# Kernel tuning notes

Measured on AMD Instinct MI355X. Metric: run time of the kernel, lower is better.

## Reference

```python
import jax, jax.numpy as jnp
import numpy as np

D = 1024
H = 16
HD = D // H
EPS = 1e-8


def setup_inputs() -> dict:
    key = jax.random.key(0)
    ks = jax.random.split(key, 12)
    B, S = 2, 2048
    scale = 1.0 / np.sqrt(D)
    inp = {
        "x": jax.random.normal(ks[0], (B, S, D), dtype=jnp.float32),
        "M": jax.random.uniform(ks[1], (B, S, S), dtype=jnp.float32),
        "Wq": jax.random.normal(ks[2], (D, D), dtype=jnp.float32) * scale,
        "bq": jax.random.normal(ks[3], (D,), dtype=jnp.float32) * 0.01,
        "Wk": jax.random.normal(ks[4], (D, D), dtype=jnp.float32) * scale,
        "bk": jax.random.normal(ks[5], (D,), dtype=jnp.float32) * 0.01,
        "Wv": jax.random.normal(ks[6], (D, D), dtype=jnp.float32) * scale,
        "bv": jax.random.normal(ks[7], (D,), dtype=jnp.float32) * 0.01,
        "Wo": jax.random.normal(ks[8], (D, D), dtype=jnp.float32) * scale,
        "bo": jax.random.normal(ks[9], (D,), dtype=jnp.float32) * 0.01,
    }
    return inp


def reference(x, M, Wq, bq, Wk, bk, Wv, bv, Wo, bo):
    B, S, _ = x.shape
    sm_scale = HD ** -0.5
    # projections (torch Linear: x @ W^T + b), split into heads: [B,H,S,HD]
    def proj(W, b):
        return (x @ W.T + b).reshape(B, S, H, HD).transpose(0, 2, 1, 3)
    Q, K, V = proj(Wq, bq), proj(Wk, bk), proj(Wv, bv)
    # scores: [B,H,S,S], gated pre-softmax by M broadcast over heads
    scores = jnp.einsum("bhqd,bhkd->bhqk", Q, K) * sm_scale
    Mb = M[:, None, :, :]  # [B,1,S,S]
    scores = scores * Mb
    attn = jax.nn.softmax(scores, axis=-1)
    # post-softmax re-gate + L1 renormalize
    A_sparse = attn * Mb
    norm = jnp.sum(jnp.abs(A_sparse), axis=-1, keepdims=True) + EPS
    A_bar = A_sparse / norm
    out = jnp.einsum("bhqk,bhkd->bhqd", A_bar, V)
    out = out.transpose(0, 2, 1, 3).reshape(B, S, D)
    return out @ Wo.T + bo
```

## Files before the change

### kernel.cpp

```cpp
#include <hip/hip_runtime.h>
#include <hip/hip_bf16.h>
#include <stdint.h>

#define S_LEN 2048
#define D_DIM 1024
#define NROW 4096

typedef __attribute__((ext_vector_type(8))) short short8;
typedef __attribute__((ext_vector_type(4))) float f32x4;
typedef __attribute__((ext_vector_type(4))) int i32x4;
typedef __attribute__((ext_vector_type(8))) _Float16 h8;
typedef unsigned short ushort_t;

__device__ __forceinline__ ushort_t f2bf(float f) {
  uint32_t u = __float_as_uint(f);
  u += 0x7fffu + ((u >> 16) & 1u);
  return (ushort_t)(u >> 16);
}

__device__ __forceinline__ ushort_t f2h(float f) {
  _Float16 h = (_Float16)f;
  return __builtin_bit_cast(ushort_t, h);
}

__device__ __forceinline__ void gload16(const void* g, void* l) {
  __builtin_amdgcn_global_load_lds((const __attribute__((address_space(1))) void*)g,
                                   (__attribute__((address_space(3))) void*)l, 16, 0, 0);
}

__global__ void convert4_kernel(const float* __restrict__ x,
                                const float* __restrict__ wq, const float* __restrict__ wk,
                                const float* __restrict__ wv,
                                ushort_t* __restrict__ xb, ushort_t* __restrict__ wcat) {
  const float* src; ushort_t* dst; int n;
  switch (blockIdx.y) {
    case 0: src = x;  dst = xb;             n = NROW * D_DIM;  break;
    case 1: src = wq; dst = wcat;           n = D_DIM * D_DIM; break;
    case 2: src = wk; dst = wcat + 1048576; n = D_DIM * D_DIM; break;
    default: src = wv; dst = wcat + 2097152; n = D_DIM * D_DIM; break;
  }
  int base = (blockIdx.x * 256 + threadIdx.x) * 8;
  if (base >= n) return;
  f32x4 va = *(const f32x4*)(src + base);
  f32x4 vb = *(const f32x4*)(src + base + 4);
  short8 o;
  o[0] = (short)f2bf(va[0]); o[1] = (short)f2bf(va[1]);
  o[2] = (short)f2bf(va[2]); o[3] = (short)f2bf(va[3]);
  o[4] = (short)f2bf(vb[0]); o[5] = (short)f2bf(vb[1]);
  o[6] = (short)f2bf(vb[2]); o[7] = (short)f2bf(vb[3]);
  *(short8*)(dst + base) = o;
}

__global__ void convert_wo_kernel(const float* __restrict__ wo, ushort_t* __restrict__ wob) {
  int base = (blockIdx.x * 256 + threadIdx.x) * 8;
  f32x4 va = *(const f32x4*)(wo + base);
  f32x4 vb = *(const f32x4*)(wo + base + 4);
  short8 o;
  o[0] = (short)f2bf(va[0]); o[1] = (short)f2bf(va[1]);
  o[2] = (short)f2bf(va[2]); o[3] = (short)f2bf(va[3]);
  o[4] = (short)f2bf(vb[0]); o[5] = (short)f2bf(vb[1]);
  o[6] = (short)f2bf(vb[2]); o[7] = (short)f2bf(vb[3]);
  *(short8*)(wob + base) = o;
}

__global__ __launch_bounds__(256) void m2_transform(const float* __restrict__ M,
                                                    ushort_t* __restrict__ M2) {
  int tid = blockIdx.x * 256 + threadIdx.x;
  int lane = tid & 63, w = (tid >> 6) & 7, kt = (tid >> 9) & 31, combo = tid >> 14;
  int c0 = lane & 15, g = lane >> 4;
  int b = combo >> 4, q0i = combo & 15;
  const float* src = M + ((size_t)b * 2048 + q0i * 128 + w * 16 + c0) * 2048 + kt * 64 + g * 4;
  ushort_t outv[16];
#pragma unroll
  for (int nf = 0; nf < 4; ++nf) {
    f32x4 v = *(const f32x4*)(src + nf * 16);
#pragma unroll
    for (int r = 0; r < 4; ++r)
      outv[nf * 4 + r] = f2h(v[r]);
  }
  *(short8*)(M2 + (size_t)tid * 16)     = *(short8*)&outv[0];
  *(short8*)(M2 + (size_t)tid * 16 + 8) = *(short8*)&outv[8];
}

template<int MODE>
__global__ __launch_bounds__(256, 4) void gemm_glds(const ushort_t* __restrict__ A,
                                                    const ushort_t* __restrict__ Bw,
                                                    const float* __restrict__ bias0,
                                                    const float* __restrict__ bias1,
                                                    const float* __restrict__ bias2,
                                                    void* __restrict__ Cout) {
  __shared__ ushort_t As[128 * 64];
  __shared__ ushort_t Bs[128 * 64];
  const int t = threadIdx.x;
  const int lane = t & 63;
  const int w = t >> 6;
  const int wm = w >> 1, wn = w & 1;
  const int m0 = blockIdx.x * 128, n0 = blockIdx.y * 128;
  const int g = lane >> 4, c0 = lane & 15;
  const int srow = lane >> 3, scol = (lane & 7) * 8;

  f32x4 acc[4][4] = {};

  for (int kt = 0; kt < 16; ++kt) {
    const int kk = kt * 64;
#pragma unroll
    for (int i = 0; i < 4; ++i) {
      gload16(A  + (size_t)(m0 + w * 32 + i * 8 + srow) * D_DIM + kk + scol, &As[(w * 32 + i * 8) * 64]);
      gload16(Bw + (size_t)(n0 + w * 32 + i * 8 + srow) * D_DIM + kk + scol, &Bs[(w * 32 + i * 8) * 64]);
    }
    asm volatile("s_waitcnt vmcnt(0)" ::: "memory");
    __syncthreads();
#pragma unroll
    for (int kc = 0; kc < 2; ++kc) {
      short8 af[4], bf[4];
#pragma unroll
      for (int mf = 0; mf < 4; ++mf)
        af[mf] = *(const short8*)&As[(wm * 64 + mf * 16 + c0) * 64 + kc * 32 + g * 8];
#pragma unroll
      for (int nf = 0; nf < 4; ++nf)
        bf[nf] = *(const short8*)&Bs[(wn * 64 + nf * 16 + c0) * 64 + kc * 32 + g * 8];
#pragma unroll
      for (int mf = 0; mf < 4; ++mf)
#pragma unroll
        for (int nf = 0; nf < 4; ++nf)
          acc[mf][nf] = __builtin_amdgcn_mfma_f32_16x16x32_bf16(af[mf], bf[nf], acc[mf][nf], 0, 0, 0);
    }
    __syncthreads();
  }

#pragma unroll
  for (int nf = 0; nf < 4; ++nf) {
    int jj = n0 + wn * 64 + nf * 16 + c0;
    float bval;
    if (MODE == 0) {
      int proj = jj >> 10, jcol = jj & 1023;
      const float* bp = (proj == 0) ? bias0 : ((proj == 1) ? bias1 : bias2);
      bval = bp[jcol];
    } else {
      bval = bias0[jj];
    }
#pragma unroll
    for (int mf = 0; mf < 4; ++mf) {
#pragma unroll
      for (int r = 0; r < 4; ++r) {
        int ii = m0 + wm * 64 + mf * 16 + g * 4 + r;
        float v = acc[mf][nf][r] + bval;
        if (MODE == 2) {
          ((float*)Cout)[(size_t)ii * D_DIM + jj] = v;
        } else {
          int proj = jj >> 10, jcol = jj & 1023;
          if (proj == 0) v *= 0.125f;
          int bb = ii >> 11, s = ii & 2047;
          size_t addr;
          if (proj < 2) {
            int hcol = jcol >> 6, hd = jcol & 63;
            addr = (size_t)proj * 4194304 + ((size_t)(bb * 16 + hcol) * 2048 + s) * 64 + hd;
          } else {
            addr = (size_t)2 * 4194304 + ((size_t)bb * 1024 + jcol) * 2048 + s;
          }
          ((ushort_t*)Cout)[addr] = f2bf(v);
        }
      }
    }
  }
}

__global__ __launch_bounds__(512, 4) void attn_kernel(const ushort_t* __restrict__ Qg,
                                                      const ushort_t* __restrict__ Kg,
                                                      const ushort_t* __restrict__ Vtg,
                                                      const ushort_t* __restrict__ M2,
                                                      ushort_t* __restrict__ aout) {
  __shared__ ushort_t Ks[2][64 * 72];
  __shared__ ushort_t Vts[2][64 * 72];

  const int t = threadIdx.x, lane = t & 63, w = t >> 6;
  const int g = lane >> 4, c0 = lane & 15;
  const int id = blockIdx.x;
  const int r8 = id & 7, hh = (id >> 3) & 15, ss = id >> 7;
  const int combo = r8 + 8 * ss, b = combo >> 4, q0 = (combo & 15) * 128;
  const int bh = b * 16 + hh;

  const ushort_t* Qbase  = Qg  + ((size_t)bh * 2048 + q0) * 64;
  const ushort_t* Kbase  = Kg  + (size_t)bh * 2048 * 64;
  const ushort_t* Vtbase = Vtg + (size_t)bh * 64 * 2048;
  const ushort_t* M2base = M2 + ((size_t)combo * 32 * 8 + w) * 64 * 16 + (size_t)lane * 16;

  short8 qf[2];
#pragma unroll
  for (int kc = 0; kc < 2; ++kc)
    qf[kc] = *(const short8*)(Qbase + (size_t)(w * 16 + c0) * 64 + kc * 32 + g * 8);

  f32x4 o[4] = {};
  float dpe = 0.f;
  const int idxA = (((g & 1) * 2 + (g >> 1)) * 16 + c0) * 4;
  const int idxB = (((g & 1) * 2 + 1 - (g >> 1)) * 16 + c0) * 4;
  const bool glo = (g < 2);
  const bool gb = (g & 1);

  const int srow = t >> 3, sc8 = (t & 7) * 8;
  short8 rk, rv, rm0, rm1, rm0n, rm1n;

  rk  = *(const short8*)(Kbase + (size_t)srow * 64 + sc8);
  rv  = *(const short8*)(Vtbase + (size_t)srow * 2048 + sc8);
  rm0 = *(const short8*)(M2base);
  rm1 = *(const short8*)(M2base + 8);
  *(short8*)&Ks[0][srow * 72 + sc8]  = rk;
  *(short8*)&Vts[0][srow * 72 + sc8] = rv;
  __syncthreads();

  for (int kt = 0; kt < 32; ++kt) {
    const int cur = kt & 1;
    if (kt < 31) {
      const int k0 = (kt + 1) * 64;
      rk  = *(const short8*)(Kbase + (size_t)(k0 + srow) * 64 + sc8);
      rv  = *(const short8*)(Vtbase + (size_t)srow * 2048 + k0 + sc8);
      rm0n = *(const short8*)(M2base + (size_t)(kt + 1) * 8192);
      rm1n = *(const short8*)(M2base + (size_t)(kt + 1) * 8192 + 8);
    }

    f32x4 sf[4] = {};
#pragma unroll
    for (int kc = 0; kc < 2; ++kc) {
      short8 kf[4];
#pragma unroll
      for (int nf = 0; nf < 4; ++nf)
        kf[nf] = *(const short8*)&Ks[cur][(nf * 16 + c0) * 72 + kc * 32 + g * 8];
#pragma unroll
      for (int nf = 0; nf < 4; ++nf)
        sf[nf] = __builtin_amdgcn_mfma_f32_16x16x32_bf16(kf[nf], qf[kc], sf[nf], 0, 0, 0);
    }

    h8 mh0 = __builtin_bit_cast(h8, rm0);
    h8 mh1 = __builtin_bit_cast(h8, rm1);
    uint32_t w4[4][2];
#pragma unroll
    for (int nf = 0; nf < 4; ++nf) {
      float p[4];
#pragma unroll
      for (int r = 0; r < 4; ++r) {
        float m = (nf < 2) ? (float)mh0[nf * 4 + r] : (float)mh1[(nf - 2) * 4 + r];
        float e = __expf(sf[nf][r] * m);
        float pe = m * e;
        dpe += pe;
        p[r] = pe;
      }
      asm("v_cvt_pk_bf16_f32 %0, %1, %2" : "=v"(w4[nf][0]) : "v"(p[0]), "v"(p[1]));
      asm("v_cvt_pk_bf16_f32 %0, %1, %2" : "=v"(w4[nf][1]) : "v"(p[2]), "v"(p[3]));
    }

    short8 pf[2];
#pragma unroll
    for (int kc = 0; kc < 2; ++kc) {
      uint32_t sA0 = gb ? w4[2 * kc + 1][0] : w4[2 * kc][0];
      uint32_t sA1 = gb ? w4[2 * kc + 1][1] : w4[2 * kc][1];
      uint32_t sB0 = gb ? w4[2 * kc][0]     : w4[2 * kc + 1][0];
      uint32_t sB1 = gb ? w4[2 * kc][1]     : w4[2 * kc + 1][1];
      uint32_t rA0 = (uint32_t)__builtin_amdgcn_ds_bpermute(idxA, (int)sA0);
      uint32_t rA1 = (uint32_t)__builtin_amdgcn_ds_bpermute(idxA, (int)sA1);
      uint32_t rB0 = (uint32_t)__builtin_amdgcn_ds_bpermute(idxB, (int)sB0);
      uint32_t rB1 = (uint32_t)__builtin_amdgcn_ds_bpermute(idxB, (int)sB1);
      i32x4 f4;
      f4[0] = (int)(glo ? rA0 : rB0);
      f4[1] = (int)(glo ? rA1 : rB1);
      f4[2] = (int)(glo ? rB0 : rA0);
      f4[3] = (int)(glo ? rB1 : rA1);
      pf[kc] = __builtin_bit_cast(short8, f4);
    }

#pragma unroll
    for (int kc = 0; kc < 2; ++kc) {
#pragma unroll
      for (int df = 0; df < 4; ++df) {
        short8 vf = *(const short8*)&Vts[cur][(df * 16 + c0) * 72 + kc * 32 + g * 8];
        o[df] = __builtin_amdgcn_mfma_f32_16x16x32_bf16(vf, pf[kc], o[df], 0, 0, 0);
      }
    }

    if (kt < 31) {
      *(short8*)&Ks[cur ^ 1][srow * 72 + sc8]  = rk;
      *(short8*)&Vts[cur ^ 1][srow * 72 + sc8] = rv;
      rm0 = rm0n; rm1 = rm1n;
    }
    __syncthreads();
  }

  dpe += __shfl_xor(dpe, 16);
  dpe += __shfl_xor(dpe, 32);
  float inv = 1.0f / dpe;

#pragma unroll
  for (int df = 0; df < 4; ++df) {
    float v0 = o[df][0] * inv, v1 = o[df][1] * inv;
    float v2 = o[df][2] * inv, v3 = o[df][3] * inv;
    uint32_t d0, d1;
    asm("v_cvt_pk_bf16_f32 %0, %1, %2" : "=v"(d0) : "v"(v0), "v"(v1));
    asm("v_cvt_pk_bf16_f32 %0, %1, %2" : "=v"(d1) : "v"(v2), "v"(v3));
    unsigned long long pk = (unsigned long long)d0 | ((unsigned long long)d1 << 32);
    *(unsigned long long*)&aout[((size_t)b * 2048 + q0 + w * 16 + c0) * 1024 + hh * 64 + df * 16 + g * 4] = pk;
  }
}

extern "C" void kernel_launch(void* const* d_in, const int* in_sizes, int n_in,
                              void* d_out, int out_size, void* d_ws, size_t ws_size,
                              hipStream_t stream) {
  const float* x  = (const float*)d_in[0];
  const float* M  = (const float*)d_in[1];
  const float* Wq = (const float*)d_in[2];
  const float* bq = (const float*)d_in[3];
  const float* Wk = (const float*)d_in[4];
  const float* bk = (const float*)d_in[5];
  const float* Wv = (const float*)d_in[6];
  const float* bv = (const float*)d_in[7];
  const float* Wo = (const float*)d_in[8];
  const float* bo = (const float*)d_in[9];
  float* out = (float*)d_out;
  char* ws = (char*)d_ws;

  ushort_t* Qb    = (ushort_t*)(ws);
  ushort_t* Kb    = (ushort_t*)(ws + 8388608);
  ushort_t* Vtb   = (ushort_t*)(ws + 16777216);
  ushort_t* xb    = (ushort_t*)(ws + 25165824);
  ushort_t* Wcat  = (ushort_t*)(ws + 33554432);
  ushort_t* M2    = (ushort_t*)(ws + 25165824);
  ushort_t* aoutb = (ushort_t*)(ws + 41943040);
  ushort_t* wob   = (ushort_t*)(ws);

  convert4_kernel<<<dim3(2048, 4), 256, 0, stream>>>(x, Wq, Wk, Wv, xb, Wcat);
  gemm_glds<0><<<dim3(32, 24), 256, 0, stream>>>(xb, Wcat, bq, bk, bv, (void*)Qb);
  m2_transform<<<2048, 256, 0, stream>>>(M, M2);
  attn_kernel<<<512, 512, 0, stream>>>(Qb, Kb, Vtb, M2, aoutb);
  convert_wo_kernel<<<512, 256, 0, stream>>>(Wo, wob);
  gemm_glds<2><<<dim3(32, 8), 256, 0, stream>>>(aoutb, wob, bo, bo, bo, (void*)out);
}
```

Measured before the change: 151.9 us.

## Fuse mask conversion into attention and shrink attention blocks to 64 query rows

Drops the separate m2_transform kernel that converted M to fp16 in a fragment-friendly layout. The attention kernel now reads fp32 M directly per key tile. The attention grid is re-tiled from 512 blocks of 512 threads (128 query rows) to 1024 blocks of 256 threads (64 query rows), and the K/V shared buffer goes from double-buffered to single-buffered with an extra barrier. The intent is to remove one kernel launch plus the write and re-read of M2, and to raise occupancy. The cost is that every head block re-reads the full fp32 M row from memory (16 heads reuse it, hopefully from L2), and single buffering may serialize loads and compute.

```diff
diff --git a/kernel.cpp b/kernel.cpp
--- a/kernel.cpp
+++ b/kernel.cpp
@@ -9,18 +9,12 @@
 typedef __attribute__((ext_vector_type(8))) short short8;
 typedef __attribute__((ext_vector_type(4))) float f32x4;
 typedef __attribute__((ext_vector_type(4))) int i32x4;
-typedef __attribute__((ext_vector_type(8))) _Float16 h8;
 typedef unsigned short ushort_t;
 
 __device__ __forceinline__ ushort_t f2bf(float f) {
   uint32_t u = __float_as_uint(f);
   u += 0x7fffu + ((u >> 16) & 1u);
   return (ushort_t)(u >> 16);
-}
-
-__device__ __forceinline__ ushort_t f2h(float f) {
-  _Float16 h = (_Float16)f;
-  return __builtin_bit_cast(ushort_t, h);
 }
 
 __device__ __forceinline__ void gload16(const void* g, void* l) {
@@ -61,25 +55,6 @@
   o[4] = (short)f2bf(vb[0]); o[5] = (short)f2bf(vb[1]);
   o[6] = (short)f2bf(vb[2]); o[7] = (short)f2bf(vb[3]);
   *(short8*)(wob + base) = o;
-}
-
-__global__ __launch_bounds__(256) void m2_transform(const float* __restrict__ M,
-                                                    ushort_t* __restrict__ M2) {
-  int tid = blockIdx.x * 256 + threadIdx.x;
-  int lane = tid & 63, w = (tid >> 6) & 7, kt = (tid >> 9) & 31, combo = tid >> 14;
-  int c0 = lane & 15, g = lane >> 4;
-  int b = combo >> 4, q0i = combo & 15;
-  const float* src = M + ((size_t)b * 2048 + q0i * 128 + w * 16 + c0) * 2048 + kt * 64 + g * 4;
-  ushort_t outv[16];
-#pragma unroll
-  for (int nf = 0; nf < 4; ++nf) {
-    f32x4 v = *(const f32x4*)(src + nf * 16);
-#pragma unroll
-    for (int r = 0; r < 4; ++r)
-      outv[nf * 4 + r] = f2h(v[r]);
-  }
-  *(short8*)(M2 + (size_t)tid * 16)     = *(short8*)&outv[0];
-  *(short8*)(M2 + (size_t)tid * 16 + 8) = *(short8*)&outv[8];
 }
 
 template<int MODE>
@@ -165,25 +140,27 @@
   }
 }
 
-__global__ __launch_bounds__(512, 4) void attn_kernel(const ushort_t* __restrict__ Qg,
+__global__ __launch_bounds__(256, 4) void attn_kernel(const ushort_t* __restrict__ Qg,
                                                       const ushort_t* __restrict__ Kg,
                                                       const ushort_t* __restrict__ Vtg,
-                                                      const ushort_t* __restrict__ M2,
+                                                      const float* __restrict__ Mg,
                                                       ushort_t* __restrict__ aout) {
-  __shared__ ushort_t Ks[2][64 * 72];
-  __shared__ ushort_t Vts[2][64 * 72];
+  __shared__ ushort_t Ks[64 * 72];
+  __shared__ ushort_t Vts[64 * 72];
 
   const int t = threadIdx.x, lane = t & 63, w = t >> 6;
   const int g = lane >> 4, c0 = lane & 15;
   const int id = blockIdx.x;
-  const int r8 = id & 7, hh = (id >> 3) & 15, ss = id >> 7;
-  const int combo = r8 + 8 * ss, b = combo >> 4, q0 = (combo & 15) * 128;
+  const int xcd = id & 7, j = id >> 3;
+  const int hh = j & 15, gi = j >> 4;
+  const int g64 = xcd + 8 * gi;
+  const int b = g64 >> 5, q0 = (g64 & 31) * 64;
   const int bh = b * 16 + hh;
 
   const ushort_t* Qbase  = Qg  + ((size_t)bh * 2048 + q0) * 64;
   const ushort_t* Kbase  = Kg  + (size_t)bh * 2048 * 64;
   const ushort_t* Vtbase = Vtg + (size_t)bh * 64 * 2048;
-  const ushort_t* M2base = M2 + ((size_t)combo * 32 * 8 + w) * 64 * 16 + (size_t)lane * 16;
+  const float*    Mbase  = Mg + ((size_t)b * 2048 + q0 + w * 16 + c0) * 2048 + g * 4;
 
   short8 qf[2];
 #pragma unroll
@@ -197,25 +174,27 @@
   const bool glo = (g < 2);
   const bool gb = (g & 1);
 
-  const int srow = t >> 3, sc8 = (t & 7) * 8;
-  short8 rk, rv, rm0, rm1, rm0n, rm1n;
-
-  rk  = *(const short8*)(Kbase + (size_t)srow * 64 + sc8);
-  rv  = *(const short8*)(Vtbase + (size_t)srow * 2048 + sc8);
-  rm0 = *(const short8*)(M2base);
-  rm1 = *(const short8*)(M2base + 8);
-  *(short8*)&Ks[0][srow * 72 + sc8]  = rk;
-  *(short8*)&Vts[0][srow * 72 + sc8] = rv;
-  __syncthreads();
+  short8 rk[2], rv[2];
+#define A_LOAD(kt) { const int k0 = (kt) * 64; \
+    _Pragma("unroll") for (int i = 0; i < 2; ++i) { int c = i * 256 + t; int row = c >> 3, c8 = (c & 7) * 8; \
+      rk[i] = *(const short8*)(Kbase  + (size_t)(k0 + row) * 64 + c8); \
+      rv[i] = *(const short8*)(Vtbase + (size_t)row * 2048 + k0 + c8); } }
+#define A_WRITE() { \
+    _Pragma("unroll") for (int i = 0; i < 2; ++i) { int c = i * 256 + t; int row = c >> 3, c8 = (c & 7) * 8; \
+      *(short8*)&Ks[row * 72 + c8]  = rk[i]; \
+      *(short8*)&Vts[row * 72 + c8] = rv[i]; } }
+
+  A_LOAD(0); A_WRITE(); __syncthreads();
 
   for (int kt = 0; kt < 32; ++kt) {
-    const int cur = kt & 1;
-    if (kt < 31) {
-      const int k0 = (kt + 1) * 64;
-      rk  = *(const short8*)(Kbase + (size_t)(k0 + srow) * 64 + sc8);
-      rv  = *(const short8*)(Vtbase + (size_t)srow * 2048 + k0 + sc8);
-      rm0n = *(const short8*)(M2base + (size_t)(kt + 1) * 8192);
-      rm1n = *(const short8*)(M2base + (size_t)(kt + 1) * 8192 + 8);
+    if (kt < 31) A_LOAD(kt + 1);
+
+    f32x4 mv[4];
+    {
+      const float* Mk = Mbase + kt * 64;
+#pragma unroll
+      for (int nf = 0; nf < 4; ++nf)
+        mv[nf] = *(const f32x4*)(Mk + nf * 16);
     }
 
     f32x4 sf[4] = {};
@@ -224,21 +203,19 @@
       short8 kf[4];
 #pragma unroll
       for (int nf = 0; nf < 4; ++nf)
-        kf[nf] = *(const short8*)&Ks[cur][(nf * 16 + c0) * 72 + kc * 32 + g * 8];
+        kf[nf] = *(const short8*)&Ks[(nf * 16 + c0) * 72 + kc * 32 + g * 8];
 #pragma unroll
       for (int nf = 0; nf < 4; ++nf)
         sf[nf] = __builtin_amdgcn_mfma_f32_16x16x32_bf16(kf[nf], qf[kc], sf[nf], 0, 0, 0);
     }
 
-    h8 mh0 = __builtin_bit_cast(h8, rm0);
-    h8 mh1 = __builtin_bit_cast(h8, rm1);
     uint32_t w4[4][2];
 #pragma unroll
     for (int nf = 0; nf < 4; ++nf) {
       float p[4];
 #pragma unroll
       for (int r = 0; r < 4; ++r) {
-        float m = (nf < 2) ? (float)mh0[nf * 4 + r] : (float)mh1[(nf - 2) * 4 + r];
+        float m = mv[nf][r];
         float e = __expf(sf[nf][r] * m);
         float pe = m * e;
         dpe += pe;
@@ -271,17 +248,16 @@
     for (int kc = 0; kc < 2; ++kc) {
 #pragma unroll
       for (int df = 0; df < 4; ++df) {
-        short8 vf = *(const short8*)&Vts[cur][(df * 16 + c0) * 72 + kc * 32 + g * 8];
+        short8 vf = *(const short8*)&Vts[(df * 16 + c0) * 72 + kc * 32 + g * 8];
         o[df] = __builtin_amdgcn_mfma_f32_16x16x32_bf16(vf, pf[kc], o[df], 0, 0, 0);
       }
     }
 
+    __syncthreads();
     if (kt < 31) {
-      *(short8*)&Ks[cur ^ 1][srow * 72 + sc8]  = rk;
-      *(short8*)&Vts[cur ^ 1][srow * 72 + sc8] = rv;
-      rm0 = rm0n; rm1 = rm1n;
-    }
-    __syncthreads();
+      A_WRITE();
+      __syncthreads();
+    }
   }
 
   dpe += __shfl_xor(dpe, 16);
@@ -298,6 +274,8 @@
     unsigned long long pk = (unsigned long long)d0 | ((unsigned long long)d1 << 32);
     *(unsigned long long*)&aout[((size_t)b * 2048 + q0 + w * 16 + c0) * 1024 + hh * 64 + df * 16 + g * 4] = pk;
   }
+#undef A_LOAD
+#undef A_WRITE
 }
 
 extern "C" void kernel_launch(void* const* d_in, const int* in_sizes, int n_in,
@@ -321,14 +299,12 @@
   ushort_t* Vtb   = (ushort_t*)(ws + 16777216);
   ushort_t* xb    = (ushort_t*)(ws + 25165824);
   ushort_t* Wcat  = (ushort_t*)(ws + 33554432);
-  ushort_t* M2    = (ushort_t*)(ws + 25165824);
   ushort_t* aoutb = (ushort_t*)(ws + 41943040);
-  ushort_t* wob   = (ushort_t*)(ws);
+  ushort_t* wob   = (ushort_t*)(ws + 39845888);
 
   convert4_kernel<<<dim3(2048, 4), 256, 0, stream>>>(x, Wq, Wk, Wv, xb, Wcat);
+  convert_wo_kernel<<<512, 256, 0, stream>>>(Wo, wob);
   gemm_glds<0><<<dim3(32, 24), 256, 0, stream>>>(xb, Wcat, bq, bk, bv, (void*)Qb);
-  m2_transform<<<2048, 256, 0, stream>>>(M, M2);
-  attn_kernel<<<512, 512, 0, stream>>>(Qb, Kb, Vtb, M2, aoutb);
-  convert_wo_kernel<<<512, 256, 0, stream>>>(Wo, wob);
+  attn_kernel<<<1024, 256, 0, stream>>>(Qb, Kb, Vtb, M, aoutb);
   gemm_glds<2><<<dim3(32, 8), 256, 0, stream>>>(aoutb, wob, bo, bo, bo, (void*)out);
 }
```

Result: slower. 158.4 us (+4.3%).

## Process two K/V tiles per iteration with four-slot LDS ring buffer

Applied to the files above, without the earlier changes.

The attention loop now processes two 64-key tiles per iteration. It uses a four-slot LDS ring and prefetches the next two tiles' K, V and mask into registers. This halves the number of block barriers and deepens the prefetch. In exchange it doubles LDS use per block and raises register pressure, which can lower the number of resident blocks per CU. An unused COMPUTE_TILE macro is also defined.

```diff
diff --git a/kernel.cpp b/kernel.cpp
--- a/kernel.cpp
+++ b/kernel.cpp
@@ -170,8 +170,8 @@
                                                       const ushort_t* __restrict__ Vtg,
                                                       const ushort_t* __restrict__ M2,
                                                       ushort_t* __restrict__ aout) {
-  __shared__ ushort_t Ks[2][64 * 72];
-  __shared__ ushort_t Vts[2][64 * 72];
+  __shared__ ushort_t Ks[4][64 * 72];
+  __shared__ ushort_t Vts[4][64 * 72];
 
   const int t = threadIdx.x, lane = t & 63, w = t >> 6;
   const int g = lane >> 4, c0 = lane & 15;
@@ -198,88 +198,151 @@
   const bool gb = (g & 1);
 
   const int srow = t >> 3, sc8 = (t & 7) * 8;
-  short8 rk, rv, rm0, rm1, rm0n, rm1n;
-
-  rk  = *(const short8*)(Kbase + (size_t)srow * 64 + sc8);
-  rv  = *(const short8*)(Vtbase + (size_t)srow * 2048 + sc8);
-  rm0 = *(const short8*)(M2base);
-  rm1 = *(const short8*)(M2base + 8);
-  *(short8*)&Ks[0][srow * 72 + sc8]  = rk;
-  *(short8*)&Vts[0][srow * 72 + sc8] = rv;
+
+#define COMPUTE_TILE(bidx, RM0, RM1) { \
+    f32x4 sf[4] = {}; \
+    _Pragma("unroll") for (int kc = 0; kc < 2; ++kc) { \
+      short8 kf[4]; \
+      _Pragma("unroll") for (int nf = 0; nf < 4; ++nf) \
+        kf[nf] = *(const short8*)&Ks[bidx][(nf * 16 + c0) * 72 + kc * 32 + g * 8]; \
+      _Pragma("unroll") for (int nf = 0; nf < 4; ++nf) \
+        sf[nf] = __builtin_amdgcn_mfma_f32_16x16x32_bf16(kf[nf], qf[kc], sf[nf], 0, 0, 0); \
+    } \
+    h8 mh0 = __builtin_bit_cast(h8, RM0); \
+    h8 mh1 = __builtin_bit_cast(h8, RM1); \
+    uint32_t w4[4][2]; \
+    _Pragma("unroll") for (int nf = 0; nf < 4; ++nf) { \
+      float p[4]; \
+      _Pragma("unroll") for (int r = 0; r < 4; ++r) { \
+        float m = (nf < 2) ? (float)mh0[nf * 4 + r] : (float)mh1[(nf - 2) * 4 + r]; \
+        float e = __expf(sf[nf][r] * m); \
+        float pe = m * e; \
+        dpe += pe; \
+        p[r] = pe; \
+      } \
+      asm("v_cvt_pk_bf16_f32 %0, %1, %2" : "=v"(w4[nf][0]) : "v"(p[0]), "v"(p[1])); \
+      asm("v_cvt_pk_bf16_f32 %0, %1, %2" : "=v"(w4[nf][1]) : "v"(p[2]), "v"(p[3])); \
+    } \
+    short8 pf[2]; \
+    _Pragma("unroll") for (int kc = 0; kc < 2; ++kc) { \
+      uint32_t sA0 = gb ? w4[2 * kc + 1][0] : w4[2 * kc][0]; \
+      uint32_t sA1 = gb ? w4[2 * kc + 1][1] : w4[2 * kc][1]; \
+      uint32_t sB0 = gb ? w4[2 * kc][0]     : w4[2 * kc + 1][0]; \
+      uint32_t sB1 = gb ? w4[2 * kc][1]     : w4[2 * kc + 1][1]; \
+      uint32_t rA0 = (uint32_t)__builtin_amdgcn_ds_bpermute(idxA, (int)sA0); \
+      uint32_t rA1 = (uint32_t)__builtin_amdgcn_ds_bpermute(idxA, (int)sA1); \
+      uint32_t rB0 = (uint32_t)__builtin_amdgcn_ds_bpermute(idxB, (int)sB0); \
+      uint32_t rB1 = (uint32_t)__builtin_amdgcn_ds_bpermute(idxB, (int)sB1); \
+      i32x4 f4; \
+      f4[0] = (int)(glo ? rA0 : rB0); \
+      f4[1] = (int)(glo ? rA1 : rB1); \
+      f4[2] = (int)(glo ? rB0 : rA0); \
+      f4[3] = (int)(glo ? rB1 : rA1); \
+      pf[kc] = __builtin_bit_cast(short8, f4); \
+    } \
+    _Pragma("unroll") for (int kc = 0; kc < 2; ++kc) { \
+      _Pragma("unroll") for (int df = 0; df < 4; ++df) { \
+        short8 vf = *(const short8*)&Vts[bidx][(df * 16 + c0) * 72 + kc * 32 + g * 8]; \
+        o[df] = __builtin_amdgcn_mfma_f32_16x16x32_bf16(vf, pf[kc], o[df], 0, 0, 0); \
+      } \
+    } }
+
+  short8 rmA0, rmA1, rmB0, rmB1;
+  {
+    short8 k0 = *(const short8*)(Kbase + (size_t)srow * 64 + sc8);
+    short8 v0 = *(const short8*)(Vtbase + (size_t)srow * 2048 + sc8);
+    short8 k1 = *(const short8*)(Kbase + (size_t)(64 + srow) * 64 + sc8);
+    short8 v1 = *(const short8*)(Vtbase + (size_t)srow * 2048 + 64 + sc8);
+    *(short8*)&Ks[0][srow * 72 + sc8]  = k0;
+    *(short8*)&Vts[0][srow * 72 + sc8] = v0;
+    *(short8*)&Ks[1][srow * 72 + sc8]  = k1;
+    *(short8*)&Vts[1][srow * 72 + sc8] = v1;
+    rmA0 = *(const short8*)(M2base);
+    rmA1 = *(const short8*)(M2base + 8);
+    rmB0 = *(const short8*)(M2base + 8192);
+    rmB1 = *(const short8*)(M2base + 8192 + 8);
+  }
   __syncthreads();
 
-  for (int kt = 0; kt < 32; ++kt) {
-    const int cur = kt & 1;
-    if (kt < 31) {
-      const int k0 = (kt + 1) * 64;
-      rk  = *(const short8*)(Kbase + (size_t)(k0 + srow) * 64 + sc8);
-      rv  = *(const short8*)(Vtbase + (size_t)srow * 2048 + k0 + sc8);
-      rm0n = *(const short8*)(M2base + (size_t)(kt + 1) * 8192);
-      rm1n = *(const short8*)(M2base + (size_t)(kt + 1) * 8192 + 8);
-    }
-
-    f32x4 sf[4] = {};
-#pragma unroll
-    for (int kc = 0; kc < 2; ++kc) {
-      short8 kf[4];
-#pragma unroll
-      for (int nf = 0; nf < 4; ++nf)
-        kf[nf] = *(const short8*)&Ks[cur][(nf * 16 + c0) * 72 + kc * 32 + g * 8];
-#pragma unroll
-      for (int nf = 0; nf < 4; ++nf)
-        sf[nf] = __builtin_amdgcn_mfma_f32_16x16x32_bf16(kf[nf], qf[kc], sf[nf], 0, 0, 0);
-    }
-
-    h8 mh0 = __builtin_bit_cast(h8, rm0);
-    h8 mh1 = __builtin_bit_cast(h8, rm1);
-    uint32_t w4[4][2];
-#pragma unroll
-    for (int nf = 0; nf < 4; ++nf) {
-      float p[4];
-#pragma unroll
-      for (int r = 0; r < 4; ++r) {
-        float m = (nf < 2) ? (float)mh0[nf * 4 + r] : (float)mh1[(nf - 2) * 4 + r];
-        float e = __expf(sf[nf][r] * m);
-        float pe = m * e;
-        dpe += pe;
-        p[r] = pe;
-      }
-      asm("v_cvt_pk_bf16_f32 %0, %1, %2" : "=v"(w4[nf][0]) : "v"(p[0]), "v"(p[1]));
-      asm("v_cvt_pk_bf16_f32 %0, %1, %2" : "=v"(w4[nf][1]) : "v"(p[2]), "v"(p[3]));
-    }
-
-    short8 pf[2];
-#pragma unroll
-    for (int kc = 0; kc < 2; ++kc) {
-      uint32_t sA0 = gb ? w4[2 * kc + 1][0] : w4[2 * kc][0];
-      uint32_t sA1 = gb ? w4[2 * kc + 1][1] : w4[2 * kc][1];
-      uint32_t sB0 = gb ? w4[2 * kc][0]     : w4[2 * kc + 1][0];
-      uint32_t sB1 = gb ? w4[2 * kc][1]     : w4[2 * kc + 1][1];
-      uint32_t rA0 = (uint32_t)__builtin_amdgcn_ds_bpermute(idxA, (int)sA0);
-      uint32_t rA1 = (uint32_t)__builtin_amdgcn_ds_bpermute(idxA, (int)sA1);
-      uint32_t rB0 = (uint32_t)__builtin_amdgcn_ds_bpermute(idxB, (int)sB0);
-      uint32_t rB1 = (uint32_t)__builtin_amdgcn_ds_bpermute(idxB, (int)sB1);
-      i32x4 f4;
-      f4[0] = (int)(glo ? rA0 : rB0);
-      f4[1] = (int)(glo ? rA1 : rB1);
-      f4[2] = (int)(glo ? rB0 : rA0);
-      f4[3] = (int)(glo ? rB1 : rA1);
-      pf[kc] = __builtin_bit_cast(short8, f4);
-    }
-
-#pragma unroll
-    for (int kc = 0; kc < 2; ++kc) {
-#pragma unroll
-      for (int df = 0; df < 4; ++df) {
-        short8 vf = *(const short8*)&Vts[cur][(df * 16 + c0) * 72 + kc * 32 + g * 8];
-        o[df] = __builtin_amdgcn_mfma_f32_16x16x32_bf16(vf, pf[kc], o[df], 0, 0, 0);
-      }
-    }
-
-    if (kt < 31) {
-      *(short8*)&Ks[cur ^ 1][srow * 72 + sc8]  = rk;
-      *(short8*)&Vts[cur ^ 1][srow * 72 + sc8] = rv;
-      rm0 = rm0n; rm1 = rm1n;
+  for (int kt = 0; kt < 32; kt += 2) {
+    short8 rk2, rv2, rk3, rv3, rmA0n, rmA1n, rmB0n, rmB1n;
+    if (kt < 30) {
+      const int k2 = (kt + 2) * 64, k3 = (kt + 3) * 64;
+      rk2 = *(const short8*)(Kbase + (size_t)(k2 + srow) * 64 + sc8);
+      rv2 = *(const short8*)(Vtbase + (size_t)srow * 2048 + k2 + sc8);
+      rk3 = *(const short8*)(Kbase + (size_t)(k3 + srow) * 64 + sc8);
+      rv3 = *(const short8*)(Vtbase + (size_t)srow * 2048 + k3 + sc8);
+      rmA0n = *(const short8*)(M2base + (size_t)(kt + 2) * 8192);
+      rmA1n = *(const short8*)(M2base + (size_t)(kt + 2) * 8192 + 8);
+      rmB0n = *(const short8*)(M2base + (size_t)(kt + 3) * 8192);
+      rmB1n = *(const short8*)(M2base + (size_t)(kt + 3) * 8192 + 8);
+    }
+
+    ushort_t* KsA = &Ks[kt & 3][0];
+    ushort_t* VtA = &Vts[kt & 3][0];
+    ushort_t* KsB = &Ks[(kt + 1) & 3][0];
+    ushort_t* VtB = &Vts[(kt + 1) & 3][0];
+#define COMPUTE_TILE_P(KP, VP, RM0, RM1) { \
+    f32x4 sf[4] = {}; \
+    _Pragma("unroll") for (int kc = 0; kc < 2; ++kc) { \
+      short8 kf[4]; \
+      _Pragma("unroll") for (int nf = 0; nf < 4; ++nf) \
+        kf[nf] = *(const short8*)&KP[(nf * 16 + c0) * 72 + kc * 32 + g * 8]; \
+      _Pragma("unroll") for (int nf = 0; nf < 4; ++nf) \
+        sf[nf] = __builtin_amdgcn_mfma_f32_16x16x32_bf16(kf[nf], qf[kc], sf[nf], 0, 0, 0); \
+    } \
+    h8 mh0 = __builtin_bit_cast(h8, RM0); \
+    h8 mh1 = __builtin_bit_cast(h8, RM1); \
+    uint32_t w4[4][2]; \
+    _Pragma("unroll") for (int nf = 0; nf < 4; ++nf) { \
+      float p[4]; \
+      _Pragma("unroll") for (int r = 0; r < 4; ++r) { \
+        float m = (nf < 2) ? (float)mh0[nf * 4 + r] : (float)mh1[(nf - 2) * 4 + r]; \
+        float e = __expf(sf[nf][r] * m); \
+        float pe = m * e; \
+        dpe += pe; \
+        p[r] = pe; \
+      } \
+      asm("v_cvt_pk_bf16_f32 %0, %1, %2" : "=v"(w4[nf][0]) : "v"(p[0]), "v"(p[1])); \
+      asm("v_cvt_pk_bf16_f32 %0, %1, %2" : "=v"(w4[nf][1]) : "v"(p[2]), "v"(p[3])); \
+    } \
+    short8 pf[2]; \
+    _Pragma("unroll") for (int kc = 0; kc < 2; ++kc) { \
+      uint32_t sA0 = gb ? w4[2 * kc + 1][0] : w4[2 * kc][0]; \
+      uint32_t sA1 = gb ? w4[2 * kc + 1][1] : w4[2 * kc][1]; \
+      uint32_t sB0 = gb ? w4[2 * kc][0]     : w4[2 * kc + 1][0]; \
+      uint32_t sB1 = gb ? w4[2 * kc][1]     : w4[2 * kc + 1][1]; \
+      uint32_t rA0 = (uint32_t)__builtin_amdgcn_ds_bpermute(idxA, (int)sA0); \
+      uint32_t rA1 = (uint32_t)__builtin_amdgcn_ds_bpermute(idxA, (int)sA1); \
+      uint32_t rB0 = (uint32_t)__builtin_amdgcn_ds_bpermute(idxB, (int)sB0); \
+      uint32_t rB1 = (uint32_t)__builtin_amdgcn_ds_bpermute(idxB, (int)sB1); \
+      i32x4 f4; \
+      f4[0] = (int)(glo ? rA0 : rB0); \
+      f4[1] = (int)(glo ? rA1 : rB1); \
+      f4[2] = (int)(glo ? rB0 : rA0); \
+      f4[3] = (int)(glo ? rB1 : rA1); \
+      pf[kc] = __builtin_bit_cast(short8, f4); \
+    } \
+    _Pragma("unroll") for (int kc = 0; kc < 2; ++kc) { \
+      _Pragma("unroll") for (int df = 0; df < 4; ++df) { \
+        short8 vf = *(const short8*)&VP[(df * 16 + c0) * 72 + kc * 32 + g * 8]; \
+        o[df] = __builtin_amdgcn_mfma_f32_16x16x32_bf16(vf, pf[kc], o[df], 0, 0, 0); \
+      } \
+    } }
+
+    COMPUTE_TILE_P(KsA, VtA, rmA0, rmA1);
+    COMPUTE_TILE_P(KsB, VtB, rmB0, rmB1);
+
+    if (kt < 30) {
+      ushort_t* KsC = &Ks[(kt + 2) & 3][0];
+      ushort_t* VtC = &Vts[(kt + 2) & 3][0];
+      ushort_t* KsD = &Ks[(kt + 3) & 3][0];
+      ushort_t* VtD = &Vts[(kt + 3) & 3][0];
+      *(short8*)&KsC[srow * 72 + sc8] = rk2;
+      *(short8*)&VtC[srow * 72 + sc8] = rv2;
+      *(short8*)&KsD[srow * 72 + sc8] = rk3;
+      *(short8*)&VtD[srow * 72 + sc8] = rv3;
+      rmA0 = rmA0n; rmA1 = rmA1n; rmB0 = rmB0n; rmB1 = rmB1n;
     }
     __syncthreads();
   }
@@ -298,6 +361,8 @@
     unsigned long long pk = (unsigned long long)d0 | ((unsigned long long)d1 << 32);
     *(unsigned long long*)&aout[((size_t)b * 2048 + q0 + w * 16 + c0) * 1024 + hh * 64 + df * 16 + g * 4] = pk;
   }
+#undef COMPUTE_TILE
+#undef COMPUTE_TILE_P
 }
 
 extern "C" void kernel_launch(void* const* d_in, const int* in_sizes, int n_in,
```

After: 183.9 us. 1.21x slower.

## Software-pipeline QK^T one tile ahead with triple-buffered K/V shared memory

Applied to the files above, without the earlier changes.

Moves from double to triple buffering of the K and V tiles in shared memory and prefetches global data two tiles ahead. The QK^T MFMA for tile kt+1 is issued in the same iteration as the softmax and PV work for tile kt, so matrix ops can overlap with the exp/convert/permute work. The cost is more LDS per block (which can hurt occupancy at 4 blocks per CU) and more live registers for the extra score accumulators.

```diff
diff --git a/kernel.cpp b/kernel.cpp
--- a/kernel.cpp
+++ b/kernel.cpp
@@ -170,8 +170,8 @@
                                                       const ushort_t* __restrict__ Vtg,
                                                       const ushort_t* __restrict__ M2,
                                                       ushort_t* __restrict__ aout) {
-  __shared__ ushort_t Ks[2][64 * 72];
-  __shared__ ushort_t Vts[2][64 * 72];
+  __shared__ ushort_t Ks[3][64 * 72];
+  __shared__ ushort_t Vts[3][64 * 72];
 
   const int t = threadIdx.x, lane = t & 63, w = t >> 6;
   const int g = lane >> 4, c0 = lane & 15;
@@ -198,36 +198,64 @@
   const bool gb = (g & 1);
 
   const int srow = t >> 3, sc8 = (t & 7) * 8;
-  short8 rk, rv, rm0, rm1, rm0n, rm1n;
-
-  rk  = *(const short8*)(Kbase + (size_t)srow * 64 + sc8);
-  rv  = *(const short8*)(Vtbase + (size_t)srow * 2048 + sc8);
-  rm0 = *(const short8*)(M2base);
-  rm1 = *(const short8*)(M2base + 8);
-  *(short8*)&Ks[0][srow * 72 + sc8]  = rk;
-  *(short8*)&Vts[0][srow * 72 + sc8] = rv;
+
+  {
+    short8 k0 = *(const short8*)(Kbase + (size_t)srow * 64 + sc8);
+    short8 v0 = *(const short8*)(Vtbase + (size_t)srow * 2048 + sc8);
+    short8 k1 = *(const short8*)(Kbase + (size_t)(64 + srow) * 64 + sc8);
+    short8 v1 = *(const short8*)(Vtbase + (size_t)srow * 2048 + 64 + sc8);
+    *(short8*)&Ks[0][srow * 72 + sc8]  = k0;
+    *(short8*)&Vts[0][srow * 72 + sc8] = v0;
+    *(short8*)&Ks[1][srow * 72 + sc8]  = k1;
+    *(short8*)&Vts[1][srow * 72 + sc8] = v1;
+  }
+  short8 rm0 = *(const short8*)(M2base);
+  short8 rm1 = *(const short8*)(M2base + 8);
   __syncthreads();
 
+  f32x4 sf[4] = {};
+#pragma unroll
+  for (int kc = 0; kc < 2; ++kc) {
+    short8 kf[4];
+#pragma unroll
+    for (int nf = 0; nf < 4; ++nf)
+      kf[nf] = *(const short8*)&Ks[0][(nf * 16 + c0) * 72 + kc * 32 + g * 8];
+#pragma unroll
+    for (int nf = 0; nf < 4; ++nf)
+      sf[nf] = __builtin_amdgcn_mfma_f32_16x16x32_bf16(kf[nf], qf[kc], sf[nf], 0, 0, 0);
+  }
+
+  int bA = 0, bB = 1, bW = 2;
+
   for (int kt = 0; kt < 32; ++kt) {
-    const int cur = kt & 1;
+    short8 rk, rv, rm0n, rm1n;
+    if (kt < 30) {
+      const int k2 = (kt + 2) * 64;
+      rk = *(const short8*)(Kbase + (size_t)(k2 + srow) * 64 + sc8);
+      rv = *(const short8*)(Vtbase + (size_t)srow * 2048 + k2 + sc8);
+    }
     if (kt < 31) {
-      const int k0 = (kt + 1) * 64;
-      rk  = *(const short8*)(Kbase + (size_t)(k0 + srow) * 64 + sc8);
-      rv  = *(const short8*)(Vtbase + (size_t)srow * 2048 + k0 + sc8);
       rm0n = *(const short8*)(M2base + (size_t)(kt + 1) * 8192);
       rm1n = *(const short8*)(M2base + (size_t)(kt + 1) * 8192 + 8);
     }
 
-    f32x4 sf[4] = {};
-#pragma unroll
-    for (int kc = 0; kc < 2; ++kc) {
-      short8 kf[4];
-#pragma unroll
-      for (int nf = 0; nf < 4; ++nf)
-        kf[nf] = *(const short8*)&Ks[cur][(nf * 16 + c0) * 72 + kc * 32 + g * 8];
-#pragma unroll
-      for (int nf = 0; nf < 4; ++nf)
-        sf[nf] = __builtin_amdgcn_mfma_f32_16x16x32_bf16(kf[nf], qf[kc], sf[nf], 0, 0, 0);
+    ushort_t* KB = &Ks[bB][0];
+    ushort_t* VA = &Vts[bA][0];
+    ushort_t* KW = &Ks[bW][0];
+    ushort_t* VW = &Vts[bW][0];
+
+    f32x4 sfn[4] = {};
+    if (kt < 31) {
+#pragma unroll
+      for (int kc = 0; kc < 2; ++kc) {
+        short8 kf[4];
+#pragma unroll
+        for (int nf = 0; nf < 4; ++nf)
+          kf[nf] = *(const short8*)&KB[(nf * 16 + c0) * 72 + kc * 32 + g * 8];
+#pragma unroll
+        for (int nf = 0; nf < 4; ++nf)
+          sfn[nf] = __builtin_amdgcn_mfma_f32_16x16x32_bf16(kf[nf], qf[kc], sfn[nf], 0, 0, 0);
+      }
     }
 
     h8 mh0 = __builtin_bit_cast(h8, rm0);
@@ -271,17 +299,21 @@
     for (int kc = 0; kc < 2; ++kc) {
 #pragma unroll
       for (int df = 0; df < 4; ++df) {
-        short8 vf = *(const short8*)&Vts[cur][(df * 16 + c0) * 72 + kc * 32 + g * 8];
+        short8 vf = *(const short8*)&VA[(df * 16 + c0) * 72 + kc * 32 + g * 8];
         o[df] = __builtin_amdgcn_mfma_f32_16x16x32_bf16(vf, pf[kc], o[df], 0, 0, 0);
       }
     }
 
-    if (kt < 31) {
-      *(short8*)&Ks[cur ^ 1][srow * 72 + sc8]  = rk;
-      *(short8*)&Vts[cur ^ 1][srow * 72 + sc8] = rv;
-      rm0 = rm0n; rm1 = rm1n;
+    if (kt < 30) {
+      *(short8*)&KW[srow * 72 + sc8] = rk;
+      *(short8*)&VW[srow * 72 + sc8] = rv;
     }
     __syncthreads();
+
+#pragma unroll
+    for (int nf = 0; nf < 4; ++nf) sf[nf] = sfn[nf];
+    rm0 = rm0n; rm1 = rm1n;
+    int tmp = bA; bA = bB; bB = bW; bW = tmp;
   }
 
   dpe += __shfl_xor(dpe, 16);
```

Result: no change. 151.1 us (-0.5%).
